# Optimization experiments

Measured on AMD Instinct MI355X. Metric: run time of the kernel, lower is better.

The kernel has to match this reference:

```python
import jax, jax.numpy as jnp
import numpy as np

NCLASS = 21  # num_classes from init
EPS = 1e-6


def setup_inputs() -> dict:
    key = jax.random.key(0)
    k1, k2 = jax.random.split(key)
    feats = jax.random.normal(k1, (8, 256, 64, 64), dtype=jnp.float32)
    masks = jax.random.randint(k2, (8, 256, 256), 0, NCLASS, dtype=jnp.int32)
    return {"feats": feats, "masks": masks}


def reference(feats, masks):
    # feats: [B, C, h, w] float; masks: [B, H, W] int labels
    B, C, _, _ = feats.shape
    H, W = masks.shape[-2:]
    # F.interpolate(..., mode='bilinear', align_corners=False) == half-pixel bilinear resize
    f = jax.image.resize(feats, (B, C, H, W), method="bilinear")  # [B,C,H,W]
    f_flat = f.reshape(B, C, H * W)  # [B,C,P]

    # labels > nclass (e.g. 255 ignore) are clamped to the dump bucket `nclass`;
    # pixels with label == nclass are excluded (one_hot drops out-of-range rows).
    lbl = jnp.where(masks > NCLASS, NCLASS, masks).reshape(B, H * W)  # [B,P]
    onehot = jax.nn.one_hot(lbl, NCLASS, dtype=f.dtype)  # [B,P,K], dump bucket -> all zeros

    # segment-reduce: per-image per-class feature sums and pixel counts
    sums = jnp.einsum("bcp,bpk->bkc", f_flat, onehot)  # [B,K,C]
    counts = onehot.sum(axis=1)  # [B,K]
    per_img = sums / (counts[..., None] + EPS)  # [B,K,C]; absent classes -> ~0, matching torch loop skip
    prototypes = per_img.mean(axis=0)  # [K,C] (sum over batch / b)
    return prototypes
```

## Files before the change

kernel.cpp:

```cpp
#include <hip/hip_runtime.h>

#define NK 21
#define NC 256
#define NSRC 64
#define NOUT 256
#define NB 8
#define EPS 1e-6f

template <int R>
__global__ __launch_bounds__(256)
void proto_main(const float* __restrict__ feats,
                const int* __restrict__ masks,
                float* __restrict__ psum,
                float* __restrict__ pcnt) {
  constexpr int NS = NSRC / R;
  __shared__ __align__(16) float Wl[NK * R * 64];
  __shared__ int hist[NK];

  const int tid = threadIdx.x;
  const int strip = blockIdx.x;
  const int b = blockIdx.y;
  const int r0 = strip * R;

  for (int i = tid; i < NK * R * 64; i += 256) Wl[i] = 0.f;
  if (tid < NK) hist[tid] = 0;
  __syncthreads();

  int ylo = 4 * r0 - 2; if (ylo < 0) ylo = 0;
  int yhi = 4 * (r0 + R - 1) + 5; if (yhi > NOUT - 1) yhi = NOUT - 1;
  const int npix = (yhi - ylo + 1) * NOUT;
  const int own_lo = 4 * r0, own_hi = 4 * r0 + 4 * R;

  for (int i = tid; i < npix; i += 256) {
    const int x = i & (NOUT - 1);
    const int y = ylo + (i >> 8);
    const int lbl = masks[((size_t)b * NOUT + y) * NOUT + x];
    if ((unsigned)lbl < NK) {
      const int ry = y >> 2, py = y & 3;
      const int j0y = (py < 2) ? ry - 1 : ry;
      const float fy = (py == 0) ? 0.625f : (py == 1) ? 0.875f
                     : (py == 2) ? 0.125f : 0.375f;
      const int rx = x >> 2, px = x & 3;
      const int j0x = (px < 2) ? rx - 1 : rx;
      const float fx = (px == 0) ? 0.625f : (px == 1) ? 0.875f
                     : (px == 2) ? 0.125f : 0.375f;

      const int cx0 = (j0x < 0) ? 0 : j0x;
      const int cx1 = (j0x + 1 > NSRC - 1) ? NSRC - 1 : j0x + 1;
      const float wx0 = 1.f - fx, wx1 = fx;
      const int ry0 = (j0y < 0) ? 0 : j0y;
      const int ry1 = (j0y + 1 > NSRC - 1) ? NSRC - 1 : j0y + 1;
      const float wy0 = 1.f - fy, wy1 = fy;

      float* Wk = &Wl[lbl * (R * 64)];
      const int sr0 = ry0 - r0, sr1 = ry1 - r0;
      if (sr0 >= 0 && sr0 < R) {
        atomicAdd(&Wk[sr0 * 64 + cx0], wy0 * wx0);
        atomicAdd(&Wk[sr0 * 64 + cx1], wy0 * wx1);
      }
      if (sr1 >= 0 && sr1 < R) {
        atomicAdd(&Wk[sr1 * 64 + cx0], wy1 * wx0);
        atomicAdd(&Wk[sr1 * 64 + cx1], wy1 * wx1);
      }
      if (y >= own_lo && y < own_hi) atomicAdd(&hist[lbl], 1);
    }
  }
  __syncthreads();

  const int c = tid;
  const float4* fbase =
      (const float4*)(feats + ((size_t)(b * NC + c) << 12) + (size_t)r0 * 64);

  float acc[NK];
#pragma unroll
  for (int k = 0; k < NK; ++k) acc[k] = 0.f;

  for (int rr = 0; rr < R; ++rr) {
    float4 f[16];
#pragma unroll
    for (int j = 0; j < 16; ++j) f[j] = fbase[rr * 16 + j];
#pragma unroll
    for (int k = 0; k < NK; ++k) {
      const float4* w = (const float4*)&Wl[(k * R + rr) * 64];
      float a = acc[k];
#pragma unroll
      for (int j = 0; j < 16; ++j) {
        const float4 ww = w[j];
        a = fmaf(f[j].x, ww.x, a);
        a = fmaf(f[j].y, ww.y, a);
        a = fmaf(f[j].z, ww.z, a);
        a = fmaf(f[j].w, ww.w, a);
      }
      acc[k] = a;
    }
  }

  float* dst = psum + ((size_t)(b * NS + strip) * NK) * NC + c;
#pragma unroll
  for (int k = 0; k < NK; ++k) dst[k * NC] = acc[k];
  if (tid < NK) pcnt[(size_t)(b * NS + strip) * NK + tid] = (float)hist[tid];
}

__global__ __launch_bounds__(256)
void proto_main_atomic(const float* __restrict__ feats,
                       const int* __restrict__ masks,
                       float* __restrict__ psum,
                       float* __restrict__ pcnt) {
  constexpr int R = 2;
  __shared__ __align__(16) float Wl[NK * R * 64];
  __shared__ int hist[NK];
  const int tid = threadIdx.x;
  const int strip = blockIdx.x;
  const int b = blockIdx.y;
  const int r0 = strip * R;

  for (int i = tid; i < NK * R * 64; i += 256) Wl[i] = 0.f;
  if (tid < NK) hist[tid] = 0;
  __syncthreads();

  int ylo = 4 * r0 - 2; if (ylo < 0) ylo = 0;
  int yhi = 4 * (r0 + R - 1) + 5; if (yhi > NOUT - 1) yhi = NOUT - 1;
  const int npix = (yhi - ylo + 1) * NOUT;
  const int own_lo = 4 * r0, own_hi = 4 * r0 + 4 * R;

  for (int i = tid; i < npix; i += 256) {
    const int x = i & (NOUT - 1);
    const int y = ylo + (i >> 8);
    const int lbl = masks[((size_t)b * NOUT + y) * NOUT + x];
    if ((unsigned)lbl < NK) {
      const int ry = y >> 2, py = y & 3;
      const int j0y = (py < 2) ? ry - 1 : ry;
      const float fy = (py == 0) ? 0.625f : (py == 1) ? 0.875f
                     : (py == 2) ? 0.125f : 0.375f;
      const int rx = x >> 2, px = x & 3;
      const int j0x = (px < 2) ? rx - 1 : rx;
      const float fx = (px == 0) ? 0.625f : (px == 1) ? 0.875f
                     : (px == 2) ? 0.125f : 0.375f;
      const int cx0 = (j0x < 0) ? 0 : j0x;
      const int cx1 = (j0x + 1 > NSRC - 1) ? NSRC - 1 : j0x + 1;
      const float wx0 = 1.f - fx, wx1 = fx;
      const int ry0 = (j0y < 0) ? 0 : j0y;
      const int ry1 = (j0y + 1 > NSRC - 1) ? NSRC - 1 : j0y + 1;
      const float wy0 = 1.f - fy, wy1 = fy;
      float* Wk = &Wl[lbl * (R * 64)];
      const int sr0 = ry0 - r0, sr1 = ry1 - r0;
      if (sr0 >= 0 && sr0 < R) {
        atomicAdd(&Wk[sr0 * 64 + cx0], wy0 * wx0);
        atomicAdd(&Wk[sr0 * 64 + cx1], wy0 * wx1);
      }
      if (sr1 >= 0 && sr1 < R) {
        atomicAdd(&Wk[sr1 * 64 + cx0], wy1 * wx0);
        atomicAdd(&Wk[sr1 * 64 + cx1], wy1 * wx1);
      }
      if (y >= own_lo && y < own_hi) atomicAdd(&hist[lbl], 1);
    }
  }
  __syncthreads();

  const int c = tid;
  const float4* fbase =
      (const float4*)(feats + ((size_t)(b * NC + c) << 12) + (size_t)r0 * 64);
  float acc[NK];
#pragma unroll
  for (int k = 0; k < NK; ++k) acc[k] = 0.f;
  for (int rr = 0; rr < R; ++rr) {
    float4 f[16];
#pragma unroll
    for (int j = 0; j < 16; ++j) f[j] = fbase[rr * 16 + j];
#pragma unroll
    for (int k = 0; k < NK; ++k) {
      const float4* w = (const float4*)&Wl[(k * R + rr) * 64];
      float a = acc[k];
#pragma unroll
      for (int j = 0; j < 16; ++j) {
        const float4 ww = w[j];
        a = fmaf(f[j].x, ww.x, a);
        a = fmaf(f[j].y, ww.y, a);
        a = fmaf(f[j].z, ww.z, a);
        a = fmaf(f[j].w, ww.w, a);
      }
      acc[k] = a;
    }
  }
#pragma unroll
  for (int k = 0; k < NK; ++k)
    atomicAdd(&psum[((size_t)b * NK + k) * NC + c], acc[k]);
  if (tid < NK) atomicAdd(&pcnt[(size_t)b * NK + tid], (float)hist[tid]);
}

__global__ __launch_bounds__(256)
void proto_final(const float* __restrict__ psum,
                 const float* __restrict__ pcnt,
                 float* __restrict__ out, int ns) {
  const int k = blockIdx.x;
  const int b = blockIdx.y;
  const int c = threadIdx.x;
  float s = 0.f, cnt = 0.f;
  for (int st = 0; st < ns; ++st) {
    s += psum[((size_t)(b * ns + st) * NK + k) * NC + c];
    cnt += pcnt[(size_t)(b * ns + st) * NK + k];
  }
  atomicAdd(&out[k * NC + c], s / (cnt + EPS) * 0.125f);
}

extern "C" void kernel_launch(void* const* d_in, const int* in_sizes, int n_in,
                              void* d_out, int out_size, void* d_ws, size_t ws_size,
                              hipStream_t stream) {
  const float* feats = (const float*)d_in[0];
  const int* masks = (const int*)d_in[1];
  float* out = (float*)d_out;

  const size_t need1 = (size_t)NB * 64 * NK * (NC + 1) * 4;
  const size_t need2 = (size_t)NB * 32 * NK * (NC + 1) * 4;

  hipMemsetAsync(d_out, 0, (size_t)out_size * 4, stream);

  float* psum = (float*)d_ws;
  if (ws_size >= need1) {
    float* pcnt = psum + (size_t)NB * 64 * NK * NC;
    proto_main<1><<<dim3(64, NB), 256, 0, stream>>>(feats, masks, psum, pcnt);
    proto_final<<<dim3(NK, NB), 256, 0, stream>>>(psum, pcnt, out, 64);
  } else if (ws_size >= need2) {
    float* pcnt = psum + (size_t)NB * 32 * NK * NC;
    proto_main<2><<<dim3(32, NB), 256, 0, stream>>>(feats, masks, psum, pcnt);
    proto_final<<<dim3(NK, NB), 256, 0, stream>>>(psum, pcnt, out, 32);
  } else {
    float* pcnt = psum + (size_t)NB * NK * NC;
    hipMemsetAsync(d_ws, 0, ((size_t)NB * NK * NC + (size_t)NB * NK) * 4, stream);
    proto_main_atomic<<<dim3(32, NB), 256, 0, stream>>>(feats, masks, psum, pcnt);
    proto_final<<<dim3(NK, NB), 256, 0, stream>>>(psum, pcnt, out, 1);
  }
}
```

Measured before the change: 112.4 us.

## Split classes across grid z to double block count per source row

```diff
diff --git a/kernel.cpp b/kernel.cpp
--- a/kernel.cpp
+++ b/kernel.cpp
@@ -6,36 +6,37 @@
 #define NOUT 256
 #define NB 8
 #define EPS 1e-6f
-
-template <int R>
+#define KSPLIT 11
+
 __global__ __launch_bounds__(256)
 void proto_main(const float* __restrict__ feats,
                 const int* __restrict__ masks,
                 float* __restrict__ psum,
                 float* __restrict__ pcnt) {
-  constexpr int NS = NSRC / R;
-  __shared__ __align__(16) float Wl[NK * R * 64];
-  __shared__ int hist[NK];
+  __shared__ __align__(16) float Wl[KSPLIT * 64];
+  __shared__ int hist[KSPLIT];
 
   const int tid = threadIdx.x;
-  const int strip = blockIdx.x;
-  const int b = blockIdx.y;
-  const int r0 = strip * R;
-
-  for (int i = tid; i < NK * R * 64; i += 256) Wl[i] = 0.f;
-  if (tid < NK) hist[tid] = 0;
+  const int r0 = blockIdx.x;
+  const int b = blockIdx.y;
+  const int klo = blockIdx.z * KSPLIT;
+  const int kcnt = (klo + KSPLIT > NK) ? (NK - klo) : KSPLIT;
+
+  for (int i = tid; i < KSPLIT * 64; i += 256) Wl[i] = 0.f;
+  if (tid < KSPLIT) hist[tid] = 0;
   __syncthreads();
 
   int ylo = 4 * r0 - 2; if (ylo < 0) ylo = 0;
-  int yhi = 4 * (r0 + R - 1) + 5; if (yhi > NOUT - 1) yhi = NOUT - 1;
+  int yhi = 4 * r0 + 5; if (yhi > NOUT - 1) yhi = NOUT - 1;
   const int npix = (yhi - ylo + 1) * NOUT;
-  const int own_lo = 4 * r0, own_hi = 4 * r0 + 4 * R;
+  const int own_lo = 4 * r0, own_hi = 4 * r0 + 4;
 
   for (int i = tid; i < npix; i += 256) {
     const int x = i & (NOUT - 1);
     const int y = ylo + (i >> 8);
     const int lbl = masks[((size_t)b * NOUT + y) * NOUT + x];
-    if ((unsigned)lbl < NK) {
+    const int lk = lbl - klo;
+    if ((unsigned)lk < (unsigned)kcnt) {
       const int ry = y >> 2, py = y & 3;
       const int j0y = (py < 2) ? ry - 1 : ry;
       const float fy = (py == 0) ? 0.625f : (py == 1) ? 0.875f
@@ -52,17 +53,16 @@
       const int ry1 = (j0y + 1 > NSRC - 1) ? NSRC - 1 : j0y + 1;
       const float wy0 = 1.f - fy, wy1 = fy;
 
-      float* Wk = &Wl[lbl * (R * 64)];
-      const int sr0 = ry0 - r0, sr1 = ry1 - r0;
-      if (sr0 >= 0 && sr0 < R) {
-        atomicAdd(&Wk[sr0 * 64 + cx0], wy0 * wx0);
-        atomicAdd(&Wk[sr0 * 64 + cx1], wy0 * wx1);
-      }
-      if (sr1 >= 0 && sr1 < R) {
-        atomicAdd(&Wk[sr1 * 64 + cx0], wy1 * wx0);
-        atomicAdd(&Wk[sr1 * 64 + cx1], wy1 * wx1);
-      }
-      if (y >= own_lo && y < own_hi) atomicAdd(&hist[lbl], 1);
+      float* Wk = &Wl[lk * 64];
+      if (ry0 == r0) {
+        atomicAdd(&Wk[cx0], wy0 * wx0);
+        atomicAdd(&Wk[cx1], wy0 * wx1);
+      }
+      if (ry1 == r0) {
+        atomicAdd(&Wk[cx0], wy1 * wx0);
+        atomicAdd(&Wk[cx1], wy1 * wx1);
+      }
+      if (y >= own_lo && y < own_hi) atomicAdd(&hist[lk], 1);
     }
   }
   __syncthreads();
@@ -71,34 +71,51 @@
   const float4* fbase =
       (const float4*)(feats + ((size_t)(b * NC + c) << 12) + (size_t)r0 * 64);
 
-  float acc[NK];
-#pragma unroll
-  for (int k = 0; k < NK; ++k) acc[k] = 0.f;
-
-  for (int rr = 0; rr < R; ++rr) {
-    float4 f[16];
-#pragma unroll
-    for (int j = 0; j < 16; ++j) f[j] = fbase[rr * 16 + j];
-#pragma unroll
-    for (int k = 0; k < NK; ++k) {
-      const float4* w = (const float4*)&Wl[(k * R + rr) * 64];
-      float a = acc[k];
-#pragma unroll
-      for (int j = 0; j < 16; ++j) {
-        const float4 ww = w[j];
-        a = fmaf(f[j].x, ww.x, a);
-        a = fmaf(f[j].y, ww.y, a);
-        a = fmaf(f[j].z, ww.z, a);
-        a = fmaf(f[j].w, ww.w, a);
-      }
-      acc[k] = a;
-    }
-  }
-
-  float* dst = psum + ((size_t)(b * NS + strip) * NK) * NC + c;
-#pragma unroll
-  for (int k = 0; k < NK; ++k) dst[k * NC] = acc[k];
-  if (tid < NK) pcnt[(size_t)(b * NS + strip) * NK + tid] = (float)hist[tid];
+  float4 f[16];
+#pragma unroll
+  for (int j = 0; j < 16; ++j) f[j] = fbase[j];
+
+  float acc[KSPLIT];
+#pragma unroll
+  for (int kk = 0; kk < KSPLIT; ++kk) acc[kk] = 0.f;
+
+#pragma unroll
+  for (int kk = 0; kk < KSPLIT; ++kk) {
+    const float4* w = (const float4*)&Wl[kk * 64];
+    float a = 0.f;
+#pragma unroll
+    for (int j = 0; j < 16; ++j) {
+      const float4 ww = w[j];
+      a = fmaf(f[j].x, ww.x, a);
+      a = fmaf(f[j].y, ww.y, a);
+      a = fmaf(f[j].z, ww.z, a);
+      a = fmaf(f[j].w, ww.w, a);
+    }
+    acc[kk] = a;
+  }
+
+  float* dst = psum + ((size_t)(b * 64 + r0) * NK + klo) * NC + c;
+#pragma unroll
+  for (int kk = 0; kk < KSPLIT; ++kk)
+    if (kk < kcnt) dst[kk * NC] = acc[kk];
+  if (tid < kcnt)
+    pcnt[(size_t)(b * 64 + r0) * NK + klo + tid] = (float)hist[tid];
+}
+
+__global__ __launch_bounds__(256)
+void proto_final64(const float* __restrict__ psum,
+                   const float* __restrict__ pcnt,
+                   float* __restrict__ out) {
+  const int k = blockIdx.x;
+  const int b = blockIdx.y;
+  const int c = threadIdx.x;
+  float s = 0.f, cnt = 0.f;
+#pragma unroll
+  for (int st = 0; st < 64; ++st) {
+    s += psum[((size_t)(b * 64 + st) * NK + k) * NC + c];
+    cnt += pcnt[(size_t)(b * 64 + st) * NK + k];
+  }
+  atomicAdd(&out[k * NC + c], s / (cnt + EPS) * 0.125f);
 }
 
 __global__ __launch_bounds__(256)
@@ -189,17 +206,14 @@
 }
 
 __global__ __launch_bounds__(256)
-void proto_final(const float* __restrict__ psum,
-                 const float* __restrict__ pcnt,
-                 float* __restrict__ out, int ns) {
+void proto_final1(const float* __restrict__ psum,
+                  const float* __restrict__ pcnt,
+                  float* __restrict__ out) {
   const int k = blockIdx.x;
   const int b = blockIdx.y;
   const int c = threadIdx.x;
-  float s = 0.f, cnt = 0.f;
-  for (int st = 0; st < ns; ++st) {
-    s += psum[((size_t)(b * ns + st) * NK + k) * NC + c];
-    cnt += pcnt[(size_t)(b * ns + st) * NK + k];
-  }
+  const float s = psum[((size_t)b * NK + k) * NC + c];
+  const float cnt = pcnt[(size_t)b * NK + k];
   atomicAdd(&out[k * NC + c], s / (cnt + EPS) * 0.125f);
 }
 
@@ -211,23 +225,18 @@
   float* out = (float*)d_out;
 
   const size_t need1 = (size_t)NB * 64 * NK * (NC + 1) * 4;
-  const size_t need2 = (size_t)NB * 32 * NK * (NC + 1) * 4;
 
   hipMemsetAsync(d_out, 0, (size_t)out_size * 4, stream);
 
   float* psum = (float*)d_ws;
   if (ws_size >= need1) {
     float* pcnt = psum + (size_t)NB * 64 * NK * NC;
-    proto_main<1><<<dim3(64, NB), 256, 0, stream>>>(feats, masks, psum, pcnt);
-    proto_final<<<dim3(NK, NB), 256, 0, stream>>>(psum, pcnt, out, 64);
-  } else if (ws_size >= need2) {
-    float* pcnt = psum + (size_t)NB * 32 * NK * NC;
-    proto_main<2><<<dim3(32, NB), 256, 0, stream>>>(feats, masks, psum, pcnt);
-    proto_final<<<dim3(NK, NB), 256, 0, stream>>>(psum, pcnt, out, 32);
+    proto_main<<<dim3(64, NB, 2), 256, 0, stream>>>(feats, masks, psum, pcnt);
+    proto_final64<<<dim3(NK, NB), 256, 0, stream>>>(psum, pcnt, out);
   } else {
     float* pcnt = psum + (size_t)NB * NK * NC;
     hipMemsetAsync(d_ws, 0, ((size_t)NB * NK * NC + (size_t)NB * NK) * 4, stream);
     proto_main_atomic<<<dim3(32, NB), 256, 0, stream>>>(feats, masks, psum, pcnt);
-    proto_final<<<dim3(NK, NB), 256, 0, stream>>>(psum, pcnt, out, 1);
-  }
-}
+    proto_final1<<<dim3(NK, NB), 256, 0, stream>>>(psum, pcnt, out);
+  }
+}
```

New measurement: 226.6 us. 2.02x slower.
